# Kernel optimization log

Measured on AMD Instinct MI355X. Metric: run time of the kernel, lower is better.

## Reference

```python
import jax, jax.numpy as jnp
import numpy as np

BH = 32  # block_h
BW = 32  # block_w
M, K, N = 4096, 4096, 4096  # tokens, in_features, out_features


def setup_inputs() -> dict:
    key = jax.random.key(0)
    k1, k2, k3, k4 = jax.random.split(key, 4)
    data = jax.random.normal(k1, (M, K), dtype=jnp.float32)
    weight = jax.random.normal(k2, (N, K), dtype=jnp.float32) * 0.02
    bias = jax.random.normal(k3, (N,), dtype=jnp.float32) * 0.02
    # elementwise 0/1 mask over the weight matrix
    mask = jax.random.randint(k4, (N, K), 0, 2, dtype=jnp.int32)
    # conv bias of the 1x1-channel block-summing conv; chosen so ~half the
    # 32x32 blocks (sum ~ Binomial(1024, 0.5)) end up inactive
    conv_bias = jnp.full((1,), -512.0, dtype=jnp.float32)
    return {"data": data, "weight": weight, "bias": bias, "mask": mask,
            "conv_bias": conv_bias}


def reference(data, weight, bias, mask, conv_bias):
    n_out, n_in = weight.shape
    nH, nW = n_out // BH, n_in // BW
    # conv2d with all-ones (BH,BW) kernel, stride (BH,BW) == per-block sum + bias
    block_sum = mask.astype(jnp.float32).reshape(nH, BH, nW, BW).sum(axis=(1, 3))
    block_mask = (block_sum + conv_bias[0]) > 0  # [nH, nW] bool
    # dds matmul (trans_b=True): zero inactive weight blocks, out = data @ W^T
    w_blocks = weight.reshape(nH, BH, nW, BW)
    w_masked = (w_blocks * block_mask[:, None, :, None].astype(weight.dtype)
                ).reshape(n_out, n_in)
    out = jnp.einsum('mk,nk->mn', data, w_masked) + bias
    return out
```

## Files before the change

kernel.cpp:

```cpp
#include <hip/hip_runtime.h>
#include <hip/hip_bf16.h>
#include <stdint.h>

#define M_DIM 4096
#define N_DIM 4096
#define K_DIM 4096
#define NH 128
#define NW 128
#define NKT 64

typedef short bf16x8 __attribute__((ext_vector_type(8)));
typedef short bf16x4 __attribute__((ext_vector_type(4)));
typedef float f32x4 __attribute__((ext_vector_type(4)));

#define MFMA(a, b, c) __builtin_amdgcn_mfma_f32_16x16x32_bf16((a), (b), (c), 0, 0, 0)

__device__ __forceinline__ short f2bf(float f) {
  union { float f; unsigned u; } c; c.f = f;
  unsigned u = c.u;
  unsigned r = (u + 0x7fffu + ((u >> 16) & 1u)) >> 16;
  return (short)r;
}

__global__ __launch_bounds__(256) void k_block_mask(const int* __restrict__ mask,
                                                    const float* __restrict__ conv_bias,
                                                    int* __restrict__ bm) {
  const int bw = blockIdx.x, bh = blockIdx.y;
  const int t = threadIdx.x;
  const int row = t >> 3;
  const int c4 = (t & 7) << 2;
  const int4* p = (const int4*)(mask + (size_t)(bh * 32 + row) * K_DIM + bw * 32 + c4);
  int4 v = *p;
  int s = v.x + v.y + v.z + v.w;
#pragma unroll
  for (int off = 32; off > 0; off >>= 1) s += __shfl_down(s, off);
  __shared__ int red[4];
  if ((t & 63) == 0) red[t >> 6] = s;
  __syncthreads();
  if (t == 0) {
    float tot = (float)(red[0] + red[1] + red[2] + red[3]) + conv_bias[0];
    bm[bh * NW + bw] = (tot > 0.0f) ? 1 : 0;
  }
}

__global__ __launch_bounds__(256) void k_cvt_data(const float* __restrict__ in,
                                                  short* __restrict__ ob) {
  size_t i = (size_t)blockIdx.x * 256 + threadIdx.x;
  f32x4 v = ((const f32x4*)in)[i];
  bf16x4 o;
  o[0] = f2bf(v[0]); o[1] = f2bf(v[1]); o[2] = f2bf(v[2]); o[3] = f2bf(v[3]);
  ((bf16x4*)ob)[i] = o;
}

__global__ __launch_bounds__(256) void k_cvt_weight(const float* __restrict__ w,
                                                    const int* __restrict__ bm,
                                                    short* __restrict__ ob) {
  size_t i = (size_t)blockIdx.x * 256 + threadIdx.x;
  int n = (int)(i >> 10);
  int k = ((int)i & 1023) << 2;
  float m = bm[((n >> 5) << 7) + (k >> 5)] ? 1.0f : 0.0f;
  f32x4 v = ((const f32x4*)w)[i];
  bf16x4 o;
  o[0] = f2bf(v[0] * m); o[1] = f2bf(v[1] * m);
  o[2] = f2bf(v[2] * m); o[3] = f2bf(v[3] * m);
  ((bf16x4*)ob)[i] = o;
}

__global__ __launch_bounds__(512, 2) void k_gemm256(const short* __restrict__ Ab,
                                                    const short* __restrict__ Bb,
                                                    const float* __restrict__ bias,
                                                    float* __restrict__ out) {
  __shared__ short Asm[2][2][256][32];
  __shared__ short Bsm[2][2][256][32];

  const int tid = threadIdx.x;
  const int wid = tid >> 6, lane = tid & 63;
  const int wr = wid >> 2, wc = wid & 3;
  const int r = lane & 15, g0 = lane >> 4;
  const int gs = g0 ^ ((r >> 1) & 3);

  const int swz = (blockIdx.x & 7) * 32 + (blockIdx.x >> 3);
  const int bx = swz & 15, by = swz >> 4;
  const int rowM = by * 256, colN = bx * 256;

  const int srow = tid >> 2;
  const int sseg = (tid & 3) ^ ((tid >> 3) & 3);
  const int swave = wid * 512;

  const short* gA = Ab + (size_t)(rowM + srow) * K_DIM + sseg * 8;
  const short* gB = Bb + (size_t)(colN + srow) * K_DIM + sseg * 8;
  const size_t HOFF = (size_t)128 * K_DIM;

#define GLL(g, l)                                                            \
  __builtin_amdgcn_global_load_lds((const __attribute__((address_space(1))) void*)(g), \
                                   (__attribute__((address_space(3))) void*)(l), 16, 0, 0)
#define STA(BUF, kt, h, ks) GLL(gA + HOFF * (h) + (size_t)(kt) * 64 + (ks) * 32, \
                                &Asm[BUF][ks][(h) * 128][0] + swave)
#define STB(BUF, kt, h, ks) GLL(gB + HOFF * (h) + (size_t)(kt) * 64 + (ks) * 32, \
                                &Bsm[BUF][ks][(h) * 128][0] + swave)

#define LDA(BUF, ks, m) (*(const bf16x8*)&Asm[BUF][ks][wr * 128 + (m) * 16 + r][gs * 8])
#define LDB(BUF, ks, n) (*(const bf16x8*)&Bsm[BUF][ks][wc * 64 + (n) * 16 + r][gs * 8])

#define MF8(AR, nn, bb)                                                      \
  acc[0][nn] = MFMA(AR[0], bb, acc[0][nn]); acc[1][nn] = MFMA(AR[1], bb, acc[1][nn]); \
  acc[2][nn] = MFMA(AR[2], bb, acc[2][nn]); acc[3][nn] = MFMA(AR[3], bb, acc[3][nn]); \
  acc[4][nn] = MFMA(AR[4], bb, acc[4][nn]); acc[5][nn] = MFMA(AR[5], bb, acc[5][nn]); \
  acc[6][nn] = MFMA(AR[6], bb, acc[6][nn]); acc[7][nn] = MFMA(AR[7], bb, acc[7][nn]);

#define BAR __builtin_amdgcn_s_barrier()
#define SB0 __builtin_amdgcn_sched_barrier(0)
#define PRIO1 __builtin_amdgcn_s_setprio(1)
#define PRIO0 __builtin_amdgcn_s_setprio(0)
#define VMW_(N) asm volatile("s_waitcnt vmcnt(" #N ")" ::: "memory")
#define VMW(N) VMW_(N)

#define TILE(BUF, NB, u, SB, SA, SR, VM0, VM2)                               \
  {                                                                          \
                                               \
    BAR; SB0;                                                                \
    bB[0] = LDB(BUF, 0, 2); bB[1] = LDB(BUF, 0, 3);                          \
    aY[0] = LDA(BUF, 1, 0); aY[1] = LDA(BUF, 1, 1);                          \
    aY[2] = LDA(BUF, 1, 2); aY[3] = LDA(BUF, 1, 3);                          \
    PRIO1; MF8(aX, 0, bA[0]); MF8(aX, 1, bA[1]); PRIO0;                      \
    if (SB) { STB(NB, (u) + 1, 0, 0); STB(NB, (u) + 1, 1, 0); }              \
    VMW(VM0);                                                                \
                                               \
    BAR; SB0;                                                                \
    aY[4] = LDA(BUF, 1, 4); aY[5] = LDA(BUF, 1, 5);                          \
    aY[6] = LDA(BUF, 1, 6); aY[7] = LDA(BUF, 1, 7);                          \
    bA[0] = LDB(BUF, 1, 0); bA[1] = LDB(BUF, 1, 1);                          \
    PRIO1; MF8(aX, 2, bB[0]); MF8(aX, 3, bB[1]); PRIO0;                      \
    if (SB) { STB(NB, (u) + 1, 0, 1); STB(NB, (u) + 1, 1, 1); }              \
                                               \
    BAR; SB0;                                                                \
    bB[0] = LDB(BUF, 1, 2); bB[1] = LDB(BUF, 1, 3);                          \
    PRIO1; MF8(aY, 0, bA[0]); MF8(aY, 1, bA[1]); PRIO0;                      \
    if (SA) { STA(BUF, (u) + 2, 0, 0); STA(BUF, (u) + 2, 1, 0); }            \
    VMW(VM2);                                                                \
       \
    BAR; SB0;                                                                \
    if (SR) {                                                                \
      aX[0] = LDA(NB, 0, 0); aX[1] = LDA(NB, 0, 1);                          \
      aX[2] = LDA(NB, 0, 2); aX[3] = LDA(NB, 0, 3);                          \
      aX[4] = LDA(NB, 0, 4); aX[5] = LDA(NB, 0, 5);                          \
      aX[6] = LDA(NB, 0, 6); aX[7] = LDA(NB, 0, 7);                          \
      bA[0] = LDB(NB, 0, 0); bA[1] = LDB(NB, 0, 1);                          \
    }                                                                        \
    PRIO1; MF8(aY, 2, bB[0]); MF8(aY, 3, bB[1]); PRIO0;                      \
    if (SA) { STA(BUF, (u) + 2, 0, 1); STA(BUF, (u) + 2, 1, 1); }            \
  }

  f32x4 acc[8][4];
#pragma unroll
  for (int m = 0; m < 8; ++m)
#pragma unroll
    for (int n = 0; n < 4; ++n) acc[m][n] = (f32x4){0.f, 0.f, 0.f, 0.f};

  bf16x8 aX[8], aY[8], bA[2], bB[2];

  STA(0, 0, 0, 0); STA(0, 0, 1, 0); STA(0, 0, 0, 1); STA(0, 0, 1, 1);
  STB(0, 0, 0, 0); STB(0, 0, 1, 0); STB(0, 0, 0, 1); STB(0, 0, 1, 1);
  STA(1, 1, 0, 0); STA(1, 1, 1, 0); STA(1, 1, 0, 1); STA(1, 1, 1, 1);
  VMW(4);
  BAR; SB0;
  aX[0] = LDA(0, 0, 0); aX[1] = LDA(0, 0, 1); aX[2] = LDA(0, 0, 2);
  aX[3] = LDA(0, 0, 3); aX[4] = LDA(0, 0, 4); aX[5] = LDA(0, 0, 5);
  aX[6] = LDA(0, 0, 6); aX[7] = LDA(0, 0, 7);
  bA[0] = LDB(0, 0, 0); bA[1] = LDB(0, 0, 1);

#pragma unroll 1
  for (int u = 0; u < NKT - 2; u += 2) {
    TILE(0, 1, u, 1, 1, 1, 6, 4);
    TILE(1, 0, u + 1, 1, 1, 1, 6, 4);
  }
  TILE(0, 1, NKT - 2, 1, 0, 1, 6, 2);
  TILE(1, 0, NKT - 1, 0, 0, 0, 0, 0);

  const int orow = rowM + wr * 128;
  const int ocol = colN + wc * 64;
#pragma unroll
  for (int n = 0; n < 4; ++n) {
    int col = ocol + n * 16 + r;
    float bz = bias[col];
#pragma unroll
    for (int m = 0; m < 8; ++m) {
      int row0 = orow + m * 16 + g0 * 4;
#pragma unroll
      for (int j = 0; j < 4; ++j)
        out[(size_t)(row0 + j) * N_DIM + col] = acc[m][n][j] + bz;
    }
  }
#undef TILE
#undef GLL
#undef STA
#undef STB
#undef LDA
#undef LDB
#undef MF8
#undef BAR
#undef SB0
#undef PRIO1
#undef PRIO0
#undef VMW
#undef VMW_
}

__global__ __launch_bounds__(256) void k_naive(const float* __restrict__ A,
                                               const float* __restrict__ W,
                                               const float* __restrict__ bias,
                                               const int* __restrict__ bm,
                                               float* __restrict__ out) {
  int col = blockIdx.x * 16 + (threadIdx.x & 15);
  int row = blockIdx.y * 16 + (threadIdx.x >> 4);
  float s = 0.f;
  for (int kb = 0; kb < K_DIM / 32; ++kb) {
    if (bm[(col >> 5) * NW + kb]) {
      int kbase = kb * 32;
#pragma unroll 8
      for (int k = 0; k < 32; ++k)
        s += A[(size_t)row * K_DIM + kbase + k] * W[(size_t)col * K_DIM + kbase + k];
    }
  }
  out[(size_t)row * N_DIM + col] = s + bias[col];
}

extern "C" void kernel_launch(void* const* d_in, const int* in_sizes, int n_in,
                              void* d_out, int out_size, void* d_ws, size_t ws_size,
                              hipStream_t stream) {
  const float* data = (const float*)d_in[0];
  const float* weight = (const float*)d_in[1];
  const float* bias = (const float*)d_in[2];
  const int* mask = (const int*)d_in[3];
  const float* conv_bias = (const float*)d_in[4];
  float* out = (float*)d_out;

  int* bm = (int*)d_ws;
  const size_t off_a = 65536;
  const size_t off_b = off_a + (size_t)M_DIM * K_DIM * 2;
  const size_t needed = off_b + (size_t)N_DIM * K_DIM * 2;

  k_block_mask<<<dim3(NW, NH), 256, 0, stream>>>(mask, conv_bias, bm);

  if (ws_size >= needed) {
    short* Abf = (short*)((char*)d_ws + off_a);
    short* Wbf = (short*)((char*)d_ws + off_b);
    k_cvt_data<<<dim3((M_DIM * (K_DIM / 4)) / 256), 256, 0, stream>>>(data, Abf);
    k_cvt_weight<<<dim3((N_DIM * (K_DIM / 4)) / 256), 256, 0, stream>>>(weight, bm, Wbf);
    k_gemm256<<<dim3(256), 512, 0, stream>>>(Abf, Wbf, bias, out);
  } else {
    k_naive<<<dim3(N_DIM / 16, M_DIM / 16), 256, 0, stream>>>(data, weight, bias, bm, out);
  }
}
```

Before: 160.1 us.

## Skip MFMAs for inactive weight blocks in GEMM via wave-uniform block-mask bits

Changes the warp tiling so every wave covers all 256 output columns (8 column-blocks of 32) and 32 rows, so each 32x32 weight block maps to a wave-uniform branch. The block mask for the tile's 8 column-blocks is loaded once with ballots, and the B-fragment LDS reads and MFMAs for inactive blocks are skipped. This aims to remove about half of the matrix-core work, which the data makes inactive. The cost is more B reads per wave, branchy code inside the tightly scheduled pipeline, and more accumulator registers per wave.

```diff
diff --git a/kernel.cpp b/kernel.cpp
--- a/kernel.cpp
+++ b/kernel.cpp
@@ -69,13 +69,13 @@
 __global__ __launch_bounds__(512, 2) void k_gemm256(const short* __restrict__ Ab,
                                                     const short* __restrict__ Bb,
                                                     const float* __restrict__ bias,
+                                                    const int* __restrict__ bm,
                                                     float* __restrict__ out) {
   __shared__ short Asm[2][2][256][32];
   __shared__ short Bsm[2][2][256][32];
 
   const int tid = threadIdx.x;
   const int wid = tid >> 6, lane = tid & 63;
-  const int wr = wid >> 2, wc = wid & 3;
   const int r = lane & 15, g0 = lane >> 4;
   const int gs = g0 ^ ((r >> 1) & 3);
 
@@ -90,6 +90,27 @@
   const short* gA = Ab + (size_t)(rowM + srow) * K_DIM + sseg * 8;
   const short* gB = Bb + (size_t)(colN + srow) * K_DIM + sseg * 8;
   const size_t HOFF = (size_t)128 * K_DIM;
+
+  const int* bp = bm + (size_t)(colN >> 5) * NW;
+  unsigned long long m0l = __ballot(bp[0 * 128 + lane] != 0);
+  unsigned long long m0h = __ballot(bp[0 * 128 + 64 + lane] != 0);
+  unsigned long long m1l = __ballot(bp[1 * 128 + lane] != 0);
+  unsigned long long m1h = __ballot(bp[1 * 128 + 64 + lane] != 0);
+  unsigned long long m2l = __ballot(bp[2 * 128 + lane] != 0);
+  unsigned long long m2h = __ballot(bp[2 * 128 + 64 + lane] != 0);
+  unsigned long long m3l = __ballot(bp[3 * 128 + lane] != 0);
+  unsigned long long m3h = __ballot(bp[3 * 128 + 64 + lane] != 0);
+  unsigned long long m4l = __ballot(bp[4 * 128 + lane] != 0);
+  unsigned long long m4h = __ballot(bp[4 * 128 + 64 + lane] != 0);
+  unsigned long long m5l = __ballot(bp[5 * 128 + lane] != 0);
+  unsigned long long m5h = __ballot(bp[5 * 128 + 64 + lane] != 0);
+  unsigned long long m6l = __ballot(bp[6 * 128 + lane] != 0);
+  unsigned long long m6h = __ballot(bp[6 * 128 + 64 + lane] != 0);
+  unsigned long long m7l = __ballot(bp[7 * 128 + lane] != 0);
+  unsigned long long m7h = __ballot(bp[7 * 128 + 64 + lane] != 0);
+  __builtin_amdgcn_sched_barrier(0);
+
+#define BTJ(J, kc) ((int)((((kc) & 64) ? m##J##h : m##J##l) >> ((kc) & 63)) & 1)
 
 #define GLL(g, l)                                                            \
   __builtin_amdgcn_global_load_lds((const __attribute__((address_space(1))) void*)(g), \
@@ -99,14 +120,13 @@
 #define STB(BUF, kt, h, ks) GLL(gB + HOFF * (h) + (size_t)(kt) * 64 + (ks) * 32, \
                                 &Bsm[BUF][ks][(h) * 128][0] + swave)
 
-#define LDA(BUF, ks, m) (*(const bf16x8*)&Asm[BUF][ks][wr * 128 + (m) * 16 + r][gs * 8])
-#define LDB(BUF, ks, n) (*(const bf16x8*)&Bsm[BUF][ks][wc * 64 + (n) * 16 + r][gs * 8])
-
-#define MF8(AR, nn, bb)                                                      \
-  acc[0][nn] = MFMA(AR[0], bb, acc[0][nn]); acc[1][nn] = MFMA(AR[1], bb, acc[1][nn]); \
-  acc[2][nn] = MFMA(AR[2], bb, acc[2][nn]); acc[3][nn] = MFMA(AR[3], bb, acc[3][nn]); \
-  acc[4][nn] = MFMA(AR[4], bb, acc[4][nn]); acc[5][nn] = MFMA(AR[5], bb, acc[5][nn]); \
-  acc[6][nn] = MFMA(AR[6], bb, acc[6][nn]); acc[7][nn] = MFMA(AR[7], bb, acc[7][nn]);
+#define LDA(BUF, ks, m) (*(const bf16x8*)&Asm[BUF][ks][wid * 32 + (m) * 16 + r][gs * 8])
+#define LDB(BUF, ks, n) (*(const bf16x8*)&Bsm[BUF][ks][(n) * 16 + r][gs * 8])
+
+#define MFJ(A0, A1, B0, B1, f)                                               \
+  acc[0][f] = MFMA(A0, B0, acc[0][f]);   acc[1][f] = MFMA(A1, B0, acc[1][f]); \
+  acc[0][(f) + 1] = MFMA(A0, B1, acc[0][(f) + 1]);                           \
+  acc[1][(f) + 1] = MFMA(A1, B1, acc[1][(f) + 1]);
 
 #define BAR __builtin_amdgcn_s_barrier()
 #define SB0 __builtin_amdgcn_sched_barrier(0)
@@ -117,57 +137,94 @@
 
 #define TILE(BUF, NB, u, SB, SA, SR, VM0, VM2)                               \
   {                                                                          \
-                                               \
+    const int kb = 2 * (u);                                                  \
+    const int c0 = BTJ(0, kb), c1 = BTJ(1, kb), c2 = BTJ(2, kb), c3 = BTJ(3, kb); \
+    const int c4 = BTJ(4, kb), c5 = BTJ(5, kb), c6 = BTJ(6, kb), c7 = BTJ(7, kb); \
+    const int d0 = BTJ(0, kb + 1), d1 = BTJ(1, kb + 1), d2 = BTJ(2, kb + 1), d3 = BTJ(3, kb + 1); \
+    const int d4 = BTJ(4, kb + 1), d5 = BTJ(5, kb + 1), d6 = BTJ(6, kb + 1), d7 = BTJ(7, kb + 1); \
+                  \
     BAR; SB0;                                                                \
-    bB[0] = LDB(BUF, 0, 2); bB[1] = LDB(BUF, 0, 3);                          \
-    aY[0] = LDA(BUF, 1, 0); aY[1] = LDA(BUF, 1, 1);                          \
-    aY[2] = LDA(BUF, 1, 2); aY[3] = LDA(BUF, 1, 3);                          \
-    PRIO1; MF8(aX, 0, bA[0]); MF8(aX, 1, bA[1]); PRIO0;                      \
+    aY0 = LDA(BUF, 1, 0); aY1 = LDA(BUF, 1, 1);                              \
+    if (c4) { bB[0] = LDB(BUF, 0, 8);  bB[1] = LDB(BUF, 0, 9); }             \
+    if (c5) { bB[2] = LDB(BUF, 0, 10); bB[3] = LDB(BUF, 0, 11); }            \
+    if (c6) { bB[4] = LDB(BUF, 0, 12); bB[5] = LDB(BUF, 0, 13); }            \
+    if (c7) { bB[6] = LDB(BUF, 0, 14); bB[7] = LDB(BUF, 0, 15); }            \
+    PRIO1;                                                                   \
+    if (c0) { MFJ(aX0, aX1, bA[0], bA[1], 0) }                               \
+    if (c1) { MFJ(aX0, aX1, bA[2], bA[3], 2) }                               \
+    if (c2) { MFJ(aX0, aX1, bA[4], bA[5], 4) }                               \
+    if (c3) { MFJ(aX0, aX1, bA[6], bA[7], 6) }                               \
+    PRIO0;                                                                   \
     if (SB) { STB(NB, (u) + 1, 0, 0); STB(NB, (u) + 1, 1, 0); }              \
     VMW(VM0);                                                                \
-                                               \
+                          \
     BAR; SB0;                                                                \
-    aY[4] = LDA(BUF, 1, 4); aY[5] = LDA(BUF, 1, 5);                          \
-    aY[6] = LDA(BUF, 1, 6); aY[7] = LDA(BUF, 1, 7);                          \
-    bA[0] = LDB(BUF, 1, 0); bA[1] = LDB(BUF, 1, 1);                          \
-    PRIO1; MF8(aX, 2, bB[0]); MF8(aX, 3, bB[1]); PRIO0;                      \
+    if (d0) { bA[0] = LDB(BUF, 1, 0); bA[1] = LDB(BUF, 1, 1); }              \
+    if (d1) { bA[2] = LDB(BUF, 1, 2); bA[3] = LDB(BUF, 1, 3); }              \
+    if (d2) { bA[4] = LDB(BUF, 1, 4); bA[5] = LDB(BUF, 1, 5); }              \
+    if (d3) { bA[6] = LDB(BUF, 1, 6); bA[7] = LDB(BUF, 1, 7); }              \
+    PRIO1;                                                                   \
+    if (c4) { MFJ(aX0, aX1, bB[0], bB[1], 8) }                               \
+    if (c5) { MFJ(aX0, aX1, bB[2], bB[3], 10) }                              \
+    if (c6) { MFJ(aX0, aX1, bB[4], bB[5], 12) }                              \
+    if (c7) { MFJ(aX0, aX1, bB[6], bB[7], 14) }                              \
+    PRIO0;                                                                   \
     if (SB) { STB(NB, (u) + 1, 0, 1); STB(NB, (u) + 1, 1, 1); }              \
-                                               \
+                          \
     BAR; SB0;                                                                \
-    bB[0] = LDB(BUF, 1, 2); bB[1] = LDB(BUF, 1, 3);                          \
-    PRIO1; MF8(aY, 0, bA[0]); MF8(aY, 1, bA[1]); PRIO0;                      \
+    if (d4) { bB[0] = LDB(BUF, 1, 8);  bB[1] = LDB(BUF, 1, 9); }             \
+    if (d5) { bB[2] = LDB(BUF, 1, 10); bB[3] = LDB(BUF, 1, 11); }            \
+    if (d6) { bB[4] = LDB(BUF, 1, 12); bB[5] = LDB(BUF, 1, 13); }            \
+    if (d7) { bB[6] = LDB(BUF, 1, 14); bB[7] = LDB(BUF, 1, 15); }            \
+    PRIO1;                                                                   \
+    if (d0) { MFJ(aY0, aY1, bA[0], bA[1], 0) }                               \
+    if (d1) { MFJ(aY0, aY1, bA[2], bA[3], 2) }                               \
+    if (d2) { MFJ(aY0, aY1, bA[4], bA[5], 4) }                               \
+    if (d3) { MFJ(aY0, aY1, bA[6], bA[7], 6) }                               \
+    PRIO0;                                                                   \
     if (SA) { STA(BUF, (u) + 2, 0, 0); STA(BUF, (u) + 2, 1, 0); }            \
     VMW(VM2);                                                                \
        \
     BAR; SB0;                                                                \
     if (SR) {                                                                \
-      aX[0] = LDA(NB, 0, 0); aX[1] = LDA(NB, 0, 1);                          \
-      aX[2] = LDA(NB, 0, 2); aX[3] = LDA(NB, 0, 3);                          \
-      aX[4] = LDA(NB, 0, 4); aX[5] = LDA(NB, 0, 5);                          \
-      aX[6] = LDA(NB, 0, 6); aX[7] = LDA(NB, 0, 7);                          \
-      bA[0] = LDB(NB, 0, 0); bA[1] = LDB(NB, 0, 1);                          \
+      const int n0 = BTJ(0, kb + 2), n1 = BTJ(1, kb + 2);                    \
+      const int n2 = BTJ(2, kb + 2), n3 = BTJ(3, kb + 2);                    \
+      aX0 = LDA(NB, 0, 0); aX1 = LDA(NB, 0, 1);                              \
+      if (n0) { bA[0] = LDB(NB, 0, 0); bA[1] = LDB(NB, 0, 1); }              \
+      if (n1) { bA[2] = LDB(NB, 0, 2); bA[3] = LDB(NB, 0, 3); }              \
+      if (n2) { bA[4] = LDB(NB, 0, 4); bA[5] = LDB(NB, 0, 5); }              \
+      if (n3) { bA[6] = LDB(NB, 0, 6); bA[7] = LDB(NB, 0, 7); }              \
     }                                                                        \
-    PRIO1; MF8(aY, 2, bB[0]); MF8(aY, 3, bB[1]); PRIO0;                      \
+    PRIO1;                                                                   \
+    if (d4) { MFJ(aY0, aY1, bB[0], bB[1], 8) }                               \
+    if (d5) { MFJ(aY0, aY1, bB[2], bB[3], 10) }                              \
+    if (d6) { MFJ(aY0, aY1, bB[4], bB[5], 12) }                              \
+    if (d7) { MFJ(aY0, aY1, bB[6], bB[7], 14) }                              \
+    PRIO0;                                                                   \
     if (SA) { STA(BUF, (u) + 2, 0, 1); STA(BUF, (u) + 2, 1, 1); }            \
   }
 
-  f32x4 acc[8][4];
-#pragma unroll
-  for (int m = 0; m < 8; ++m)
-#pragma unroll
-    for (int n = 0; n < 4; ++n) acc[m][n] = (f32x4){0.f, 0.f, 0.f, 0.f};
-
-  bf16x8 aX[8], aY[8], bA[2], bB[2];
+  f32x4 acc[2][16];
+#pragma unroll
+  for (int m = 0; m < 2; ++m)
+#pragma unroll
+    for (int n = 0; n < 16; ++n) acc[m][n] = (f32x4){0.f, 0.f, 0.f, 0.f};
+
+  bf16x8 aX0, aX1, aY0, aY1, bA[8], bB[8];
 
   STA(0, 0, 0, 0); STA(0, 0, 1, 0); STA(0, 0, 0, 1); STA(0, 0, 1, 1);
   STB(0, 0, 0, 0); STB(0, 0, 1, 0); STB(0, 0, 0, 1); STB(0, 0, 1, 1);
   STA(1, 1, 0, 0); STA(1, 1, 1, 0); STA(1, 1, 0, 1); STA(1, 1, 1, 1);
   VMW(4);
   BAR; SB0;
-  aX[0] = LDA(0, 0, 0); aX[1] = LDA(0, 0, 1); aX[2] = LDA(0, 0, 2);
-  aX[3] = LDA(0, 0, 3); aX[4] = LDA(0, 0, 4); aX[5] = LDA(0, 0, 5);
-  aX[6] = LDA(0, 0, 6); aX[7] = LDA(0, 0, 7);
-  bA[0] = LDB(0, 0, 0); bA[1] = LDB(0, 0, 1);
+  {
+    const int p0 = BTJ(0, 0), p1 = BTJ(1, 0), p2 = BTJ(2, 0), p3 = BTJ(3, 0);
+    aX0 = LDA(0, 0, 0); aX1 = LDA(0, 0, 1);
+    if (p0) { bA[0] = LDB(0, 0, 0); bA[1] = LDB(0, 0, 1); }
+    if (p1) { bA[2] = LDB(0, 0, 2); bA[3] = LDB(0, 0, 3); }
+    if (p2) { bA[4] = LDB(0, 0, 4); bA[5] = LDB(0, 0, 5); }
+    if (p3) { bA[6] = LDB(0, 0, 6); bA[7] = LDB(0, 0, 7); }
+  }
 
 #pragma unroll 1
   for (int u = 0; u < NKT - 2; u += 2) {
@@ -177,14 +234,13 @@
   TILE(0, 1, NKT - 2, 1, 0, 1, 6, 2);
   TILE(1, 0, NKT - 1, 0, 0, 0, 0, 0);
 
-  const int orow = rowM + wr * 128;
-  const int ocol = colN + wc * 64;
-#pragma unroll
-  for (int n = 0; n < 4; ++n) {
-    int col = ocol + n * 16 + r;
+  const int orow = rowM + wid * 32;
+#pragma unroll
+  for (int n = 0; n < 16; ++n) {
+    int col = colN + n * 16 + r;
     float bz = bias[col];
 #pragma unroll
-    for (int m = 0; m < 8; ++m) {
+    for (int m = 0; m < 2; ++m) {
       int row0 = orow + m * 16 + g0 * 4;
 #pragma unroll
       for (int j = 0; j < 4; ++j)
@@ -197,13 +253,14 @@
 #undef STB
 #undef LDA
 #undef LDB
-#undef MF8
+#undef MFJ
 #undef BAR
 #undef SB0
 #undef PRIO1
 #undef PRIO0
 #undef VMW
 #undef VMW_
+#undef BTJ
 }
 
 __global__ __launch_bounds__(256) void k_naive(const float* __restrict__ A,
@@ -247,7 +304,7 @@
     short* Wbf = (short*)((char*)d_ws + off_b);
     k_cvt_data<<<dim3((M_DIM * (K_DIM / 4)) / 256), 256, 0, stream>>>(data, Abf);
     k_cvt_weight<<<dim3((N_DIM * (K_DIM / 4)) / 256), 256, 0, stream>>>(weight, bm, Wbf);
-    k_gemm256<<<dim3(256), 512, 0, stream>>>(Abf, Wbf, bias, out);
+    k_gemm256<<<dim3(256), 512, 0, stream>>>(Abf, Wbf, bias, bm, out);
   } else {
     k_naive<<<dim3(N_DIM / 16, M_DIM / 16), 256, 0, stream>>>(data, weight, bias, bm, out);
   }
```

New measurement: 152.4 us. 4.8% less time.
